# Optimization experiments

Hardware: AMD Instinct MI355X
Metric: run time of the kernel (lower is better)

## Reference

```python
import jax, jax.numpy as jnp
import numpy as np
from jax import lax

EPS = 1e-6
NUM_HEADS = 16
BSZ = 4


def _expected_alignment_train(p_choose):
    """p_choose: [B, T, S] -> alpha [B, T, S].
    q_ij = (1-p_{i,j-1}) q_{i,j-1} + a_{i-1,j};  a_ij = p_ij q_ij
    Per-step closed form: a_i = p_i * excl_cumprod(1-p_i) * cumsum(a_{i-1} / excl_cumprod_clamped)
    """
    B, T, S = p_choose.shape
    # safe exclusive cumprod of (1 - p) along src (fairseq exclusive_cumprod with eps clamp)
    one_minus_p = jnp.clip(1.0 - p_choose, EPS, 1.0)
    cp = jnp.cumprod(one_minus_p, axis=2)
    cumprod_1mp = jnp.concatenate([jnp.ones_like(cp[:, :, :1]), cp[:, :, :-1]], axis=2)
    cumprod_1mp_clamp = jnp.clip(cumprod_1mp, EPS, 1.0)

    init_attn = jnp.zeros((B, S), p_choose.dtype).at[:, 0].set(1.0)

    def step(prev_attn, xs):
        p_i, cp_i, cpc_i = xs  # each [B, S]
        alpha_i = jnp.clip(p_i * cp_i * jnp.cumsum(prev_attn / cpc_i, axis=1), 0.0, 1.0)
        return alpha_i, alpha_i

    xs = (jnp.swapaxes(p_choose, 0, 1),
          jnp.swapaxes(cumprod_1mp, 0, 1),
          jnp.swapaxes(cumprod_1mp_clamp, 0, 1))  # [T, B, S]
    _, alpha = lax.scan(step, init_attn, xs)
    alpha = jnp.swapaxes(alpha, 0, 1)  # [B, T, S]

    # mass preservation (no key padding): residual mass onto last source token
    residuals = 1.0 - jnp.clip(jnp.sum(alpha[:, :, :-1], axis=-1), 0.0, 1.0)
    alpha = alpha.at[:, :, -1].set(residuals)
    return alpha


def reference(q_proj, q_proj_dummy=None, *, _unused=None):
    raise NotImplementedError


def reference(q_proj, k_proj, v_proj, out_w, out_b, energy_bias):
    # q_proj/k_proj/v_proj: [bsz*num_heads, len, head_dim]
    energy = jnp.einsum('btd,bsd->bts', q_proj, k_proj) + energy_bias[0]
    p_choose = jax.nn.sigmoid(energy)                       # [B, T, S]
    alpha = _expected_alignment_train(p_choose)
    beta = alpha                                            # hard-aligned: expected_attention = alpha
    attn = jnp.einsum('bts,bsd->btd', beta, v_proj)         # [B, T, head_dim]
    BH, T, D = attn.shape
    attn = jnp.swapaxes(attn, 0, 1).reshape(T, BSZ, NUM_HEADS * D)  # [T, bsz, embed]
    out = attn @ out_w.T + out_b                            # out_proj
    return out, alpha


def setup_inputs():
    key = jax.random.key(0)
    ks = jax.random.split(key, 4)
    BH, T, S, D = 64, 1024, 1024, 64
    E = NUM_HEADS * D
    return {
        'q_proj': jax.random.normal(ks[0], (BH, T, D), jnp.float32) * 0.1,
        'k_proj': jax.random.normal(ks[1], (BH, S, D), jnp.float32) * 0.1,
        'v_proj': jax.random.normal(ks[2], (BH, S, D), jnp.float32),
        'out_w': jax.random.normal(ks[3], (E, E), jnp.float32) * 0.02,
        'out_b': jnp.zeros((E,), jnp.float32),
        'energy_bias': jnp.full((1,), -2.0, jnp.float32),
    }
```

## Files before the change

### kernel.cpp

```cpp
#include <hip/hip_runtime.h>

#define TT 1024
#define SSZ 1024
#define DD 64
#define BHN 64
#define BSZN 4
#define EEN 1024
#define EPSF 1e-6f

using f32x4 = __attribute__((ext_vector_type(4))) float;
using i32x2 = __attribute__((ext_vector_type(2))) int;
using i32x4 = __attribute__((ext_vector_type(4))) int;
using s16x8 = __attribute__((ext_vector_type(8))) short;

__device__ unsigned short g_Qb[(size_t)BHN * TT * SSZ];
__device__ unsigned short g_Pb[(size_t)BHN * TT * SSZ];
__device__ unsigned short g_Vt[(size_t)BHN * DD * SSZ];
__device__ unsigned short g_Wb[(size_t)EEN * EEN];
__device__ unsigned short g_Xb[(size_t)TT * BSZN * EEN];

template<int CTRL, int RM>
__device__ __forceinline__ float f_dpp(float x, float ident) {
  return __builtin_bit_cast(float,
      __builtin_amdgcn_update_dpp(__builtin_bit_cast(int, ident),
                                  __builtin_bit_cast(int, x),
                                  CTRL, RM, 0xF, false));
}

__device__ __forceinline__ float wscan_add(float x) {
  x += f_dpp<0x111, 0xF>(x, 0.0f);
  x += f_dpp<0x112, 0xF>(x, 0.0f);
  x += f_dpp<0x114, 0xF>(x, 0.0f);
  x += f_dpp<0x118, 0xF>(x, 0.0f);
  x += f_dpp<0x142, 0xA>(x, 0.0f);
  x += f_dpp<0x143, 0xC>(x, 0.0f);
  return x;
}

__device__ __forceinline__ float wave_shr1(float x, float ident) {
  return f_dpp<0x138, 0xF>(x, ident);
}

__device__ __forceinline__ i32x2 aload2(const unsigned short* p) {
  i32x2 r;
  asm volatile("global_load_dwordx2 %0, %1, off" : "=v"(r) : "v"(p));
  return r;
}
__device__ __forceinline__ void astore(float* p, f32x4 v) {
  asm volatile("global_store_dwordx4 %0, %1, off" :: "v"(p), "v"(v) : "memory");
}
__device__ __forceinline__ void astore2(unsigned short* p, i32x2 v) {
  asm volatile("global_store_dwordx2 %0, %1, off" :: "v"(p), "v"(v) : "memory");
}

__device__ __forceinline__ int cvt_pk(float lo, float hi) {
  int r;
  asm("v_cvt_pk_bf16_f32 %0, %1, %2" : "=v"(r) : "v"(lo), "v"(hi));
  return r;
}
__device__ __forceinline__ unsigned short bfr(float x) {
  unsigned u = __builtin_bit_cast(unsigned, x);
  u += 0x7fffu + ((u >> 16) & 1u);
  return (unsigned short)(u >> 16);
}
__device__ __forceinline__ float bfl(int u) {
  return __builtin_bit_cast(float, u << 16);
}
__device__ __forceinline__ float bfh(int u) {
  return __builtin_bit_cast(float, (int)((unsigned)u & 0xffff0000u));
}
__device__ __forceinline__ s16x8 pack8p(const float* p) {
  f32x4 a = *(const f32x4*)p;
  f32x4 b = *(const f32x4*)(p + 4);
  i32x4 r;
  r[0] = cvt_pk(a[0], a[1]); r[1] = cvt_pk(a[2], a[3]);
  r[2] = cvt_pk(b[0], b[1]); r[3] = cvt_pk(b[2], b[3]);
  return __builtin_bit_cast(s16x8, r);
}
__device__ __forceinline__ s16x8 pack8f(float v0, float v1, float v2, float v3,
                                        float v4, float v5, float v6, float v7) {
  i32x4 r;
  r[0] = cvt_pk(v0, v1); r[1] = cvt_pk(v2, v3);
  r[2] = cvt_pk(v4, v5); r[3] = cvt_pk(v6, v7);
  return __builtin_bit_cast(s16x8, r);
}

__global__ __launch_bounds__(256) void k_prep_w(const float* __restrict__ W) {
  const size_t idx = ((size_t)blockIdx.x * 256 + threadIdx.x) * 8;
  *(s16x8*)(g_Wb + idx) = pack8p(W + idx);
}

__global__ __launch_bounds__(256) void k_prep_v(const float* __restrict__ V) {
  __shared__ float tile[64][65];
  const int tid = threadIdx.x;
  const int bh = blockIdx.x >> 4;
  const int s0 = (blockIdx.x & 15) << 6;
  {
    const int r = tid >> 2, cq = (tid & 3) << 4;
    const float* src = V + ((size_t)bh * SSZ + s0 + r) * DD + cq;
    *(float4*)&tile[r][cq + 0]  = *(const float4*)(src + 0);
    *(float4*)&tile[r][cq + 4]  = *(const float4*)(src + 4);
    *(float4*)&tile[r][cq + 8]  = *(const float4*)(src + 8);
    *(float4*)&tile[r][cq + 12] = *(const float4*)(src + 12);
  }
  __syncthreads();
  {
    const int d = tid >> 2, sq = (tid & 3) << 4;
    unsigned short* dst = g_Vt + ((size_t)bh * DD + d) * SSZ + s0 + sq;
    *(s16x8*)(dst + 0) = pack8f(tile[sq + 0][d], tile[sq + 1][d], tile[sq + 2][d], tile[sq + 3][d],
                                tile[sq + 4][d], tile[sq + 5][d], tile[sq + 6][d], tile[sq + 7][d]);
    *(s16x8*)(dst + 8) = pack8f(tile[sq + 8][d], tile[sq + 9][d], tile[sq + 10][d], tile[sq + 11][d],
                                tile[sq + 12][d], tile[sq + 13][d], tile[sq + 14][d], tile[sq + 15][d]);
  }
}

__global__ __launch_bounds__(256) void k_energy(const float* __restrict__ Q,
                                                const float* __restrict__ Kp,
                                                const float* __restrict__ eb) {
  const int tid = threadIdx.x, w = tid >> 6, l = tid & 63;
  const int rl = l & 15, kg = l >> 4;
  const int bh = blockIdx.x >> 6;
  const int tile = blockIdx.x & 63;
  const int m0 = (tile >> 2) << 6;
  const int n0 = (((tile & 3) << 2) + w) << 6;
  const float* qb = Q + (size_t)bh * TT * DD;
  const float* kb = Kp + (size_t)bh * SSZ * DD;

  f32x4 acc[4][4];
#pragma unroll
  for (int i = 0; i < 4; ++i)
#pragma unroll
    for (int j = 0; j < 4; ++j) acc[i][j] = (f32x4)0.0f;

#pragma unroll
  for (int ks = 0; ks < 2; ++ks) {
    const int kof = (ks << 5) + (kg << 3);
    s16x8 af[4], bf[4];
#pragma unroll
    for (int fi = 0; fi < 4; ++fi)
      af[fi] = pack8p(qb + (size_t)(m0 + fi * 16 + rl) * DD + kof);
#pragma unroll
    for (int fj = 0; fj < 4; ++fj)
      bf[fj] = pack8p(kb + (size_t)(n0 + fj * 16 + rl) * DD + kof);
#pragma unroll
    for (int fi = 0; fi < 4; ++fi)
#pragma unroll
      for (int fj = 0; fj < 4; ++fj)
        acc[fi][fj] = __builtin_amdgcn_mfma_f32_16x16x32_bf16(af[fi], bf[fj], acc[fi][fj], 0, 0, 0);
  }

  const float bias = eb[0];
  unsigned short* pb = g_Qb + (size_t)bh * TT * SSZ;
#pragma unroll
  for (int fi = 0; fi < 4; ++fi)
#pragma unroll
    for (int r = 0; r < 4; ++r) {
      const size_t rowoff = (size_t)(m0 + fi * 16 + (kg << 2) + r) * SSZ;
#pragma unroll
      for (int fj = 0; fj < 4; ++fj) {
        float x = acc[fi][fj][r] + bias;
        float s = __builtin_amdgcn_rcpf(1.0f + __expf(-x));
        pb[rowoff + n0 + fj * 16 + rl] = bfr(s);
      }
    }
}

#define STEP(T, QS) do {                                                       \
  const int t_ = (T);                                                          \
  asm volatile("s_waitcnt vmcnt(8)" ::: "memory");                             \
  __builtin_amdgcn_sched_barrier(0);                                           \
  float fn0 = 1.0f - bfl(QS[0]);                                               \
  float fn1 = 1.0f - bfh(QS[0]);                                               \
  float fn2 = 1.0f - bfl(QS[1]);                                               \
  float fn3 = 1.0f - bfh(QS[1]);                                               \
  { int rr = t_ + 5; if (rr > TT - 1) rr = TT - 1;                             \
    QS = aload2(gqe + (size_t)rr * SSZ); }                                     \
  float ln0 = fn0, ln1 = ln0 * fn1, ln2 = ln1 * fn2, ln3 = ln2 * fn3;          \
  float An0 = ln3;                                                             \
  float An1 = An0 * f_dpp<0x111, 0xF>(An0, 1.0f);                              \
  float An2 = An1 * f_dpp<0x112, 0xF>(An1, 1.0f);                              \
  float An3 = An2 * f_dpp<0x114, 0xF>(An2, 1.0f);                              \
  float An4 = An3 * f_dpp<0x118, 0xF>(An3, 1.0f);                              \
  float An5 = An4 * f_dpp<0x142, 0xA>(An4, 1.0f);                              \
  float An6 = An5 * f_dpp<0x143, 0xC>(An5, 1.0f);                              \
  float wEn = wave_shr1(An6, 1.0f);                                            \
  float bb0 = fminf(c0  * prev0, prev0);                                       \
  float bb1 = fminf(cl0 * prev1, prev1);                                       \
  float bb2 = fminf(cl1 * prev2, prev2);                                       \
  float bb3 = fminf(cl2 * prev3, prev3);                                       \
  float Blo1 = fmaf(fc0, bb0, bb1);                                            \
  float Blo2 = fmaf(fc1, Blo1, bb2);                                           \
  float Blo3 = fmaf(fc2, Blo2, bb3);                                           \
  float B_ = fc3 * Blo3;                                                       \
  B_ = fmaf(As0, f_dpp<0x111, 0xF>(B_, 0.0f), B_);                             \
  B_ = fmaf(As1, f_dpp<0x112, 0xF>(B_, 0.0f), B_);                             \
  B_ = fmaf(As2, f_dpp<0x114, 0xF>(B_, 0.0f), B_);                             \
  B_ = fmaf(As3, f_dpp<0x118, 0xF>(B_, 0.0f), B_);                             \
  B_ = fmaf(As4, f_dpp<0x142, 0xA>(B_, 0.0f), B_);                             \
  float Bfull = fmaf(As5, f_dpp<0x143, 0xC>(B_, 0.0f), B_);                    \
  float wB = wave_shr1(Bfull, 0.0f);                                           \
  if (lane == 63) ldsAB[t_ & 1][w] = make_float2(An6, Bfull);                  \
  asm volatile("s_waitcnt lgkmcnt(0)" ::: "memory");                           \
  __builtin_amdgcn_s_barrier();                                                \
  __builtin_amdgcn_sched_barrier(0);                                           \
  float2 ab0 = ldsAB[t_ & 1][0];                                               \
  float2 ab1 = ldsAB[t_ & 1][1];                                               \
  float2 ab2 = ldsAB[t_ & 1][2];                                               \
  float Ew = 0.0f;                                                             \
  if (w == 1) Ew = ab0.y;                                                      \
  else if (w == 2) Ew = fmaf(A1g, ab0.y, ab1.y);                               \
  else if (w == 3) Ew = fmaf(A2g, fmaf(A1g, ab0.y, ab1.y), ab2.y);             \
  float El = fmaf(wE, Ew, wB);                                                 \
  float D0 = bb0 + El;                                                         \
  float D1 = fmaf(lc0, El, Blo1);                                              \
  float D2 = fmaf(lc1, El, Blo2);                                              \
  float D3 = fmaf(lc2, El, Blo3);                                              \
  float a0 = fminf(fmaf(-fc0, D0, D0), 1.0f);                                  \
  float a1 = fminf(fmaf(-fc1, D1, D1), 1.0f);                                  \
  float a2 = fminf(fmaf(-fc2, D2, D2), 1.0f);                                  \
  float a3 = fminf(fmaf(-fc3, D3, D3), 1.0f);                                  \
  prev0 = a0; prev1 = a1; prev2 = a2; prev3 = a3;                              \
  f32x4 av4; av4.x = a0; av4.y = a1; av4.z = a2; av4.w = a3;                   \
  if (tid != 255) {                                                            \
    astore(gq + (size_t)t_ * SSZ, av4);                                        \
    i32x2 pk; pk[0] = cvt_pk(a0, a1); pk[1] = cvt_pk(a2, a3);                  \
    astore2(gpb + (size_t)t_ * 32, pk);                                        \
  }                                                                            \
  float la = (a0 + a1) + (a2 + a3);                                            \
  float wsum = wscan_add(la);                                                  \
  if (lane == 63 && w < 3) ldsS[t_ & 1][w] = wsum;                             \
  if (tid == 255) {                                                            \
    if (t_ > 0) {                                                              \
      float tot = ldsS[(t_ - 1) & 1][0] + ldsS[(t_ - 1) & 1][1]                \
                + ldsS[(t_ - 1) & 1][2] + wsum_prev;                           \
      float rest = tot - pend.w;                                               \
      pend.w = 1.0f - fminf(fmaxf(rest, 0.0f), 1.0f);                          \
      astore(gq + (size_t)(t_ - 1) * SSZ, pend);                               \
      i32x2 pk2; pk2[0] = cvt_pk(pend.x, pend.y); pk2[1] = cvt_pk(pend.z, pend.w); \
      astore2(gpb + (size_t)(t_ - 1) * 32, pk2);                               \
    }                                                                          \
    pend = av4; wsum_prev = wsum;                                              \
  }                                                                            \
  fc0 = fn0; fc1 = fn1; fc2 = fn2; fc3 = fn3;                                  \
  lc0 = ln0; lc1 = ln1; lc2 = ln2;                                             \
  As0 = An0; As1 = An1; As2 = An2; As3 = An3; As4 = An4; As5 = An5;            \
  wE = wEn;                                                                    \
  float Pw_ = 1.0f;                                                            \
  if (w > 0) Pw_ = ab0.x;                                                      \
  if (w > 1) Pw_ *= ab1.x;                                                     \
  if (w > 2) Pw_ *= ab2.x;                                                     \
  c0 = (Pw_ * 1e6f) * wEn;                                                     \
  cl0 = c0 * ln0; cl1 = c0 * ln1; cl2 = c0 * ln2;                              \
  A1g = ab1.x; A2g = ab2.x;                                                    \
} while (0)

__global__ __launch_bounds__(256, 1) void k_scan(float* __restrict__ A) {
  const int b = blockIdx.x;
  const int tid = threadIdx.x;
  const int w = tid >> 6;
  const int lane = tid & 63;
  __shared__ float2 ldsAB[2][4];
  __shared__ float ldsS[2][4];

  float* gq = A + (size_t)b * TT * SSZ + ((size_t)w << 8) + ((size_t)lane << 2);
  const unsigned short* gqe = g_Qb + (size_t)b * TT * SSZ + ((size_t)w << 8) + ((size_t)lane << 2);
  const int sb = (w << 3) + (lane >> 3);
  unsigned short* gpb = g_Pb + ((size_t)(b * 32 + sb) * TT) * 32 + ((lane & 7) << 2);

  i32x2 q0 = aload2(gqe + (size_t)0 * SSZ);
  i32x2 q1 = aload2(gqe + (size_t)1 * SSZ);
  i32x2 q2 = aload2(gqe + (size_t)2 * SSZ);
  i32x2 q3 = aload2(gqe + (size_t)3 * SSZ);
  asm volatile("s_waitcnt vmcnt(0)" ::: "memory");
  __builtin_amdgcn_sched_barrier(0);

  float fc0 = 1.0f - bfl(q0[0]);
  float fc1 = 1.0f - bfh(q0[0]);
  float fc2 = 1.0f - bfl(q0[1]);
  float fc3 = 1.0f - bfh(q0[1]);
  q0 = aload2(gqe + (size_t)4 * SSZ);
  float lc0 = fc0, lc1 = lc0 * fc1, lc2 = lc1 * fc2;
  float lc3 = lc2 * fc3;
  float As0 = lc3;
  float As1 = As0 * f_dpp<0x111, 0xF>(As0, 1.0f);
  float As2 = As1 * f_dpp<0x112, 0xF>(As1, 1.0f);
  float As3 = As2 * f_dpp<0x114, 0xF>(As2, 1.0f);
  float As4 = As3 * f_dpp<0x118, 0xF>(As3, 1.0f);
  float As5 = As4 * f_dpp<0x142, 0xA>(As4, 1.0f);
  float A6  = As5 * f_dpp<0x143, 0xC>(As5, 1.0f);
  float wE = wave_shr1(A6, 1.0f);
  if (lane == 63) ldsAB[1][w] = make_float2(A6, 0.0f);
  asm volatile("s_waitcnt lgkmcnt(0)" ::: "memory");
  __builtin_amdgcn_s_barrier();
  __builtin_amdgcn_sched_barrier(0);
  float2 pab0 = ldsAB[1][0], pab1 = ldsAB[1][1], pab2 = ldsAB[1][2];
  float A1g = pab1.x, A2g = pab2.x;
  float Pw = 1.0f;
  if (w > 0) Pw = pab0.x;
  if (w > 1) Pw *= pab1.x;
  if (w > 2) Pw *= pab2.x;
  float c0 = (Pw * 1e6f) * wE;
  float cl0 = c0 * lc0, cl1 = c0 * lc1, cl2 = c0 * lc2;

  float prev0 = (tid == 0) ? 1.0f : 0.0f;
  float prev1 = 0.0f, prev2 = 0.0f, prev3 = 0.0f;
  f32x4 pend; pend.x = 0.0f; pend.y = 0.0f; pend.z = 0.0f; pend.w = 0.0f;
  float wsum_prev = 0.0f;

  for (int t0 = 0; t0 < TT; t0 += 4) {
    STEP(t0 + 0, q1);
    STEP(t0 + 1, q2);
    STEP(t0 + 2, q3);
    STEP(t0 + 3, q0);
  }

  asm volatile("s_waitcnt lgkmcnt(0)" ::: "memory");
  __builtin_amdgcn_s_barrier();
  __builtin_amdgcn_sched_barrier(0);
  if (tid == 255) {
    float tot = ldsS[(TT - 1) & 1][0] + ldsS[(TT - 1) & 1][1]
              + ldsS[(TT - 1) & 1][2] + wsum_prev;
    float rest = tot - pend.w;
    pend.w = 1.0f - fminf(fmaxf(rest, 0.0f), 1.0f);
    astore(gq + (size_t)(TT - 1) * SSZ, pend);
    i32x2 pk; pk[0] = cvt_pk(pend.x, pend.y); pk[1] = cvt_pk(pend.z, pend.w);
    astore2(gpb + (size_t)(TT - 1) * 32, pk);
  }
}

__global__ __launch_bounds__(256) void k_av() {
  const int tid = threadIdx.x, w = tid >> 6, l = tid & 63;
  const int rl = l & 15, kg = l >> 4;
  const int gw = blockIdx.x * 4 + w;
  const int bh = gw >> 6;
  const int t0 = (gw & 63) << 4;

  const unsigned short* ab = g_Pb + ((size_t)(bh * 32) * TT + (t0 + rl)) * 32 + (kg << 3);
  const unsigned short* vb = g_Vt + (size_t)bh * DD * SSZ;

  f32x4 acc[4];
#pragma unroll
  for (int j = 0; j < 4; ++j) acc[j] = (f32x4)0.0f;

  for (int kk = 0; kk < 32; ++kk) {
    const int kof = (kk << 5) + (kg << 3);
    s16x8 a = *(const s16x8*)(ab + (size_t)kk * TT * 32);
#pragma unroll
    for (int fj = 0; fj < 4; ++fj) {
      s16x8 b = *(const s16x8*)(vb + (size_t)(fj * 16 + rl) * SSZ + kof);
      acc[fj] = __builtin_amdgcn_mfma_f32_16x16x32_bf16(a, b, acc[fj], 0, 0, 0);
    }
  }

  const int bz = bh >> 4, hh = bh & 15;
#pragma unroll
  for (int fj = 0; fj < 4; ++fj) {
    const int d = fj * 16 + rl;
#pragma unroll
    for (int r = 0; r < 4; ++r) {
      const int t = t0 + (kg << 2) + r;
      g_Xb[((size_t)t * BSZN + bz) * EEN + hh * DD + d] = bfr(acc[fj][r]);
    }
  }
}

__global__ __launch_bounds__(256) void k_out(const float* __restrict__ Bb,
                                             float* __restrict__ Out) {
  const int tid = threadIdx.x, w = tid >> 6, l = tid & 63;
  const int rl = l & 15, kg = l >> 4;
  const int gw = blockIdx.x * 4 + w;
  const int m0 = (gw >> 4) << 4;
  const int n0 = (gw & 15) << 6;

  const unsigned short* xb = g_Xb + (size_t)(m0 + rl) * EEN;

  f32x4 acc[4];
#pragma unroll
  for (int j = 0; j < 4; ++j) acc[j] = (f32x4)0.0f;

  for (int kk = 0; kk < 32; ++kk) {
    const int kof = (kk << 5) + (kg << 3);
    s16x8 a = *(const s16x8*)(xb + kof);
#pragma unroll
    for (int fj = 0; fj < 4; ++fj) {
      s16x8 b = *(const s16x8*)(g_Wb + (size_t)(n0 + fj * 16 + rl) * EEN + kof);
      acc[fj] = __builtin_amdgcn_mfma_f32_16x16x32_bf16(a, b, acc[fj], 0, 0, 0);
    }
  }

#pragma unroll
  for (int fj = 0; fj < 4; ++fj) {
    const float bias = Bb[n0 + fj * 16 + rl];
#pragma unroll
    for (int r = 0; r < 4; ++r) {
      const int m = m0 + (kg << 2) + r;
      Out[(size_t)m * EEN + n0 + fj * 16 + rl] = acc[fj][r] + bias;
    }
  }
}

extern "C" void kernel_launch(void* const* d_in, const int* in_sizes, int n_in,
                              void* d_out, int out_size, void* d_ws, size_t ws_size,
                              hipStream_t stream) {
  const float* Q  = (const float*)d_in[0];
  const float* K  = (const float*)d_in[1];
  const float* V  = (const float*)d_in[2];
  const float* W  = (const float*)d_in[3];
  const float* Bb = (const float*)d_in[4];
  const float* eb = (const float*)d_in[5];
  float* Out = (float*)d_out;
  float* Alpha = Out + (size_t)TT * BSZN * EEN;

  k_prep_w<<<dim3(512), dim3(256), 0, stream>>>(W);
  k_prep_v<<<dim3(BHN * 16), dim3(256), 0, stream>>>(V);
  k_energy<<<dim3(BHN * 64), dim3(256), 0, stream>>>(Q, K, eb);
  k_scan<<<dim3(BHN), dim3(256), 0, stream>>>(Alpha);
  k_av<<<dim3(1024), dim3(256), 0, stream>>>();
  k_out<<<dim3(1024), dim3(256), 0, stream>>>(Bb, Out);
}
```

Baseline: 751.9 us.

## Pack two scan heads per block and tile V transpose into 32-wide chunks

The scan kernel now runs two heads per 512-thread block, so 32 blocks are launched instead of 64. Each 256-thread group keeps its own LDS slots, but a single block-wide barrier now synchronises both heads at every step. V is also stored transposed in 32-element source chunks (bh, chunk, d, 32), which gives k_av contiguous B-operand loads per k-step. The two-head packing couples two independent sequential scans through one barrier, which may add wait time; the benefit is unclear, since it mainly frees CUs that the short grid left idle anyway.

After: 799.1 us. 6.3% more time.

```diff
diff --git a/kernel.cpp b/kernel.cpp
--- a/kernel.cpp
+++ b/kernel.cpp
@@ -106,11 +106,13 @@
   __syncthreads();
   {
     const int d = tid >> 2, sq = (tid & 3) << 4;
-    unsigned short* dst = g_Vt + ((size_t)bh * DD + d) * SSZ + s0 + sq;
-    *(s16x8*)(dst + 0) = pack8f(tile[sq + 0][d], tile[sq + 1][d], tile[sq + 2][d], tile[sq + 3][d],
-                                tile[sq + 4][d], tile[sq + 5][d], tile[sq + 6][d], tile[sq + 7][d]);
-    *(s16x8*)(dst + 8) = pack8f(tile[sq + 8][d], tile[sq + 9][d], tile[sq + 10][d], tile[sq + 11][d],
-                                tile[sq + 12][d], tile[sq + 13][d], tile[sq + 14][d], tile[sq + 15][d]);
+    const int s1 = s0 + sq, s2 = s1 + 8;
+    unsigned short* d0 = g_Vt + ((size_t)(bh * 32 + (s1 >> 5)) * DD + d) * 32 + (s1 & 31);
+    unsigned short* d1 = g_Vt + ((size_t)(bh * 32 + (s2 >> 5)) * DD + d) * 32 + (s2 & 31);
+    *(s16x8*)d0 = pack8f(tile[sq + 0][d], tile[sq + 1][d], tile[sq + 2][d], tile[sq + 3][d],
+                         tile[sq + 4][d], tile[sq + 5][d], tile[sq + 6][d], tile[sq + 7][d]);
+    *(s16x8*)d1 = pack8f(tile[sq + 8][d], tile[sq + 9][d], tile[sq + 10][d], tile[sq + 11][d],
+                         tile[sq + 12][d], tile[sq + 13][d], tile[sq + 14][d], tile[sq + 15][d]);
   }
 }
 
@@ -199,13 +201,13 @@
   B_ = fmaf(As4, f_dpp<0x142, 0xA>(B_, 0.0f), B_);                             \
   float Bfull = fmaf(As5, f_dpp<0x143, 0xC>(B_, 0.0f), B_);                    \
   float wB = wave_shr1(Bfull, 0.0f);                                           \
-  if (lane == 63) ldsAB[t_ & 1][w] = make_float2(An6, Bfull);                  \
+  if (lane == 63) ldsAB[grp][t_ & 1][w] = make_float2(An6, Bfull);             \
   asm volatile("s_waitcnt lgkmcnt(0)" ::: "memory");                           \
   __builtin_amdgcn_s_barrier();                                                \
   __builtin_amdgcn_sched_barrier(0);                                           \
-  float2 ab0 = ldsAB[t_ & 1][0];                                               \
-  float2 ab1 = ldsAB[t_ & 1][1];                                               \
-  float2 ab2 = ldsAB[t_ & 1][2];                                               \
+  float2 ab0 = ldsAB[grp][t_ & 1][0];                                          \
+  float2 ab1 = ldsAB[grp][t_ & 1][1];                                          \
+  float2 ab2 = ldsAB[grp][t_ & 1][2];                                          \
   float Ew = 0.0f;                                                             \
   if (w == 1) Ew = ab0.y;                                                      \
   else if (w == 2) Ew = fmaf(A1g, ab0.y, ab1.y);                               \
@@ -221,18 +223,18 @@
   float a3 = fminf(fmaf(-fc3, D3, D3), 1.0f);                                  \
   prev0 = a0; prev1 = a1; prev2 = a2; prev3 = a3;                              \
   f32x4 av4; av4.x = a0; av4.y = a1; av4.z = a2; av4.w = a3;                   \
-  if (tid != 255) {                                                            \
+  if (lt != 255) {                                                             \
     astore(gq + (size_t)t_ * SSZ, av4);                                        \
     i32x2 pk; pk[0] = cvt_pk(a0, a1); pk[1] = cvt_pk(a2, a3);                  \
     astore2(gpb + (size_t)t_ * 32, pk);                                        \
   }                                                                            \
   float la = (a0 + a1) + (a2 + a3);                                            \
   float wsum = wscan_add(la);                                                  \
-  if (lane == 63 && w < 3) ldsS[t_ & 1][w] = wsum;                             \
-  if (tid == 255) {                                                            \
+  if (lane == 63 && w < 3) ldsS[grp][t_ & 1][w] = wsum;                        \
+  if (lt == 255) {                                                             \
     if (t_ > 0) {                                                              \
-      float tot = ldsS[(t_ - 1) & 1][0] + ldsS[(t_ - 1) & 1][1]                \
-                + ldsS[(t_ - 1) & 1][2] + wsum_prev;                           \
+      float tot = ldsS[grp][(t_ - 1) & 1][0] + ldsS[grp][(t_ - 1) & 1][1]      \
+                + ldsS[grp][(t_ - 1) & 1][2] + wsum_prev;                      \
       float rest = tot - pend.w;                                               \
       pend.w = 1.0f - fminf(fmaxf(rest, 0.0f), 1.0f);                          \
       astore(gq + (size_t)(t_ - 1) * SSZ, pend);                               \
@@ -254,18 +256,20 @@
   A1g = ab1.x; A2g = ab2.x;                                                    \
 } while (0)
 
-__global__ __launch_bounds__(256, 1) void k_scan(float* __restrict__ A) {
-  const int b = blockIdx.x;
+__global__ __launch_bounds__(512, 1) void k_scan(float* __restrict__ A) {
   const int tid = threadIdx.x;
-  const int w = tid >> 6;
+  const int grp = tid >> 8;
+  const int lt = tid & 255;
+  const int w = lt >> 6;
   const int lane = tid & 63;
-  __shared__ float2 ldsAB[2][4];
-  __shared__ float ldsS[2][4];
-
-  float* gq = A + (size_t)b * TT * SSZ + ((size_t)w << 8) + ((size_t)lane << 2);
-  const unsigned short* gqe = g_Qb + (size_t)b * TT * SSZ + ((size_t)w << 8) + ((size_t)lane << 2);
+  const int bh = blockIdx.x * 2 + grp;
+  __shared__ float2 ldsAB[2][2][4];
+  __shared__ float ldsS[2][2][4];
+
+  float* gq = A + (size_t)bh * TT * SSZ + ((size_t)w << 8) + ((size_t)lane << 2);
+  const unsigned short* gqe = g_Qb + (size_t)bh * TT * SSZ + ((size_t)w << 8) + ((size_t)lane << 2);
   const int sb = (w << 3) + (lane >> 3);
-  unsigned short* gpb = g_Pb + ((size_t)(b * 32 + sb) * TT) * 32 + ((lane & 7) << 2);
+  unsigned short* gpb = g_Pb + ((size_t)(bh * 32 + sb) * TT) * 32 + ((lane & 7) << 2);
 
   i32x2 q0 = aload2(gqe + (size_t)0 * SSZ);
   i32x2 q1 = aload2(gqe + (size_t)1 * SSZ);
@@ -289,11 +293,11 @@
   float As5 = As4 * f_dpp<0x142, 0xA>(As4, 1.0f);
   float A6  = As5 * f_dpp<0x143, 0xC>(As5, 1.0f);
   float wE = wave_shr1(A6, 1.0f);
-  if (lane == 63) ldsAB[1][w] = make_float2(A6, 0.0f);
+  if (lane == 63) ldsAB[grp][1][w] = make_float2(A6, 0.0f);
   asm volatile("s_waitcnt lgkmcnt(0)" ::: "memory");
   __builtin_amdgcn_s_barrier();
   __builtin_amdgcn_sched_barrier(0);
-  float2 pab0 = ldsAB[1][0], pab1 = ldsAB[1][1], pab2 = ldsAB[1][2];
+  float2 pab0 = ldsAB[grp][1][0], pab1 = ldsAB[grp][1][1], pab2 = ldsAB[grp][1][2];
   float A1g = pab1.x, A2g = pab2.x;
   float Pw = 1.0f;
   if (w > 0) Pw = pab0.x;
@@ -302,7 +306,7 @@
   float c0 = (Pw * 1e6f) * wE;
   float cl0 = c0 * lc0, cl1 = c0 * lc1, cl2 = c0 * lc2;
 
-  float prev0 = (tid == 0) ? 1.0f : 0.0f;
+  float prev0 = (lt == 0) ? 1.0f : 0.0f;
   float prev1 = 0.0f, prev2 = 0.0f, prev3 = 0.0f;
   f32x4 pend; pend.x = 0.0f; pend.y = 0.0f; pend.z = 0.0f; pend.w = 0.0f;
   float wsum_prev = 0.0f;
@@ -317,9 +321,9 @@
   asm volatile("s_waitcnt lgkmcnt(0)" ::: "memory");
   __builtin_amdgcn_s_barrier();
   __builtin_amdgcn_sched_barrier(0);
-  if (tid == 255) {
-    float tot = ldsS[(TT - 1) & 1][0] + ldsS[(TT - 1) & 1][1]
-              + ldsS[(TT - 1) & 1][2] + wsum_prev;
+  if (lt == 255) {
+    float tot = ldsS[grp][(TT - 1) & 1][0] + ldsS[grp][(TT - 1) & 1][1]
+              + ldsS[grp][(TT - 1) & 1][2] + wsum_prev;
     float rest = tot - pend.w;
     pend.w = 1.0f - fminf(fmaxf(rest, 0.0f), 1.0f);
     astore(gq + (size_t)(TT - 1) * SSZ, pend);
@@ -336,18 +340,17 @@
   const int t0 = (gw & 63) << 4;
 
   const unsigned short* ab = g_Pb + ((size_t)(bh * 32) * TT + (t0 + rl)) * 32 + (kg << 3);
-  const unsigned short* vb = g_Vt + (size_t)bh * DD * SSZ;
+  const unsigned short* vb = g_Vt + ((size_t)(bh * 32) * DD + rl) * 32 + (kg << 3);
 
   f32x4 acc[4];
 #pragma unroll
   for (int j = 0; j < 4; ++j) acc[j] = (f32x4)0.0f;
 
   for (int kk = 0; kk < 32; ++kk) {
-    const int kof = (kk << 5) + (kg << 3);
     s16x8 a = *(const s16x8*)(ab + (size_t)kk * TT * 32);
 #pragma unroll
     for (int fj = 0; fj < 4; ++fj) {
-      s16x8 b = *(const s16x8*)(vb + (size_t)(fj * 16 + rl) * SSZ + kof);
+      s16x8 b = *(const s16x8*)(vb + ((size_t)kk * DD + fj * 16) * 32);
       acc[fj] = __builtin_amdgcn_mfma_f32_16x16x32_bf16(a, b, acc[fj], 0, 0, 0);
     }
   }
@@ -414,7 +417,7 @@
   k_prep_w<<<dim3(512), dim3(256), 0, stream>>>(W);
   k_prep_v<<<dim3(BHN * 16), dim3(256), 0, stream>>>(V);
   k_energy<<<dim3(BHN * 64), dim3(256), 0, stream>>>(Q, K, eb);
-  k_scan<<<dim3(BHN), dim3(256), 0, stream>>>(Alpha);
+  k_scan<<<dim3(BHN / 2), dim3(512), 0, stream>>>(Alpha);
   k_av<<<dim3(1024), dim3(256), 0, stream>>>();
   k_out<<<dim3(1024), dim3(256), 0, stream>>>(Bb, Out);
 }
```
